# Kernel tuning notes

Measured on AMD Instinct MI355X. Metric: run time of the kernel, lower is better.

Reference implementation:

```python
import jax, jax.numpy as jnp
import numpy as np
import math

D_MODEL = 512
D_STATE = 16
D_CONV = 4
EXPAND = 2
D_INNER = D_MODEL * EXPAND
B, L = 2, 2048
EPS = 1e-8


def setup_inputs() -> dict:
    key = jax.random.key(0)
    ks = jax.random.split(key, 10)
    s_in = 1.0 / math.sqrt(D_MODEL)
    s_x = 1.0 / math.sqrt(D_INNER)
    s_c = 1.0 / math.sqrt(D_CONV)
    return {
        "x": jax.random.normal(ks[0], (B, L, D_MODEL), jnp.float32),
        "W_in": jax.random.uniform(ks[1], (D_MODEL, 2 * D_INNER), jnp.float32, -s_in, s_in),
        "b_in": jax.random.uniform(ks[2], (2 * D_INNER,), jnp.float32, -s_in, s_in),
        "conv_w": jax.random.uniform(ks[3], (D_INNER, 1, D_CONV), jnp.float32, -s_c, s_c),
        "conv_b": jax.random.uniform(ks[4], (D_INNER,), jnp.float32, -s_c, s_c),
        "W_x": jax.random.uniform(ks[5], (D_INNER, 2 * D_STATE + 1), jnp.float32, -s_x, s_x),
        "b_x": jax.random.uniform(ks[6], (2 * D_STATE + 1,), jnp.float32, -s_x, s_x),
        "A_log": jax.random.uniform(ks[7], (D_STATE,), jnp.float32, -math.log(D_STATE), -1.0),
        "D": jnp.ones((D_INNER,), jnp.float32),
        "W_out": jax.random.uniform(ks[8], (D_INNER, D_MODEL), jnp.float32, -s_x, s_x),
        "b_out": jax.random.uniform(ks[9], (D_MODEL,), jnp.float32, -s_x, s_x),
    }


def _silu(v):
    return v * jax.nn.sigmoid(v)


def _causal_depthwise_conv(x_blc, conv_w, conv_b):
    # x_blc: (B, L, D_inner); conv_w: (D_inner, 1, K). Torch pads K-1 both sides
    # then slices [:L] == causal left pad of K-1.
    lhs = jnp.transpose(x_blc, (0, 2, 1))  # (B, C, L)
    out = jax.lax.conv_general_dilated(
        lhs, conv_w,
        window_strides=(1,),
        padding=[(D_CONV - 1, 0)],
        dimension_numbers=("NCH", "OIH", "NCH"),
        feature_group_count=D_INNER,
    )
    out = out + conv_b[None, :, None]
    return jnp.transpose(out, (0, 2, 1))  # (B, L, C)


def reference(x, W_in, b_in, conv_w, conv_b, W_x, b_x, A_log, D, W_out, b_out):
    # in_proj and split
    xr = x @ W_in + b_in                      # (B, L, 2*Di)
    x_inner, res = jnp.split(xr, 2, axis=-1)  # each (B, L, Di)

    xc = _silu(_causal_depthwise_conv(x_inner, conv_w, conv_b))  # (B, L, Di)

    # selective scan (cumprod/cumsum formulation, faithful to source)
    BCdt = xc @ W_x + b_x                     # (B, L, 2S+1)
    B_sel = BCdt[..., :D_STATE]               # (B, L, S)
    C_sel = BCdt[..., D_STATE:2 * D_STATE]    # (B, L, S)
    dt = jax.nn.softplus(BCdt[..., -1:])      # (B, L, 1)

    A = -jnp.exp(A_log)                       # (S,)
    A_bar = jnp.exp(dt * A[None, None, :])    # (B, L, S)
    P = jnp.maximum(jnp.cumprod(A_bar, axis=1), EPS)  # (B, L, S)

    u = B_sel[..., None] * xc[:, :, None, :]  # (B, L, S, Di)
    g = jnp.cumsum(u / P[..., None], axis=1)  # (B, L, S, Di)
    h = g * P[..., None]                      # (B, L, S, Di)
    y = jnp.einsum("bls,blsd->bld", C_sel, h) + D[None, None, :] * xc

    y = y * _silu(res)
    return y @ W_out + b_out
```

## Files before the change

### kernel.cpp

```cpp
#include <hip/hip_runtime.h>
#include <hip/hip_bf16.h>
#include <cmath>


#define L_SEQ 2048
#define NBATCH 2
#define DI 1024
#define NC 64
#define LC 32
#define EPS_F 1e-8f
#define LOG_EPS -18.420680744f

typedef __attribute__((ext_vector_type(8))) __bf16 bf16x8;
typedef __attribute__((ext_vector_type(4))) float f32x4;

__device__ __forceinline__ float silu_f(float v) {
    return v / (1.f + __expf(-v));
}

__device__ __forceinline__ ushort bf16_bits(float v) {
    __hip_bfloat16 h = __float2bfloat16(v);
    return *reinterpret_cast<ushort*>(&h);
}

__device__ __forceinline__ float bf2f(ushort u) {
    union { unsigned u; float f; } c;
    c.u = ((unsigned)u) << 16;
    return c.f;
}

__global__ __launch_bounds__(256) void gemm1_mfma(
    const ushort* __restrict__ A, const ushort* __restrict__ Bt,
    const float* __restrict__ bias, ushort* __restrict__ C0,
    ushort* __restrict__ C1, int M, int N, int K)
{
    __shared__ ushort lA[128 * 64];
    __shared__ ushort lB[128 * 64];
    const int tid = threadIdx.x;
    const int w = tid >> 6, ln = tid & 63;
    const int wr = w >> 1, wc = w & 1;
    const int bm = blockIdx.y * 128, bn = blockIdx.x * 128;
    const int q = ln >> 4, r = ln & 15;
    f32x4 acc[4][4] = {};

    for (int k0 = 0; k0 < K; k0 += 64) {
        #pragma unroll
        for (int j = 0; j < 4; ++j) {
            int i = (w * 4 + j) * 64 + ln;
            int m = i >> 3, k8 = (i & 7) * 8;
            __builtin_amdgcn_global_load_lds(
                (const __attribute__((address_space(1))) void*)(A + (size_t)(bm + m) * K + k0 + k8),
                (__attribute__((address_space(3))) void*)(lA + (size_t)i * 8),
                16, 0, 0);
            __builtin_amdgcn_global_load_lds(
                (const __attribute__((address_space(1))) void*)(Bt + (size_t)(bn + m) * K + k0 + k8),
                (__attribute__((address_space(3))) void*)(lB + (size_t)i * 8),
                16, 0, 0);
        }
        __syncthreads();
        #pragma unroll
        for (int kk = 0; kk < 2; ++kk) {
            const int ko = kk * 32 + q * 8;
            bf16x8 af[4], bfr[4];
            #pragma unroll
            for (int m = 0; m < 4; ++m)
                af[m] = *reinterpret_cast<const bf16x8*>(&lA[(wr * 64 + m * 16 + r) * 64 + ko]);
            #pragma unroll
            for (int n = 0; n < 4; ++n)
                bfr[n] = *reinterpret_cast<const bf16x8*>(&lB[(wc * 64 + n * 16 + r) * 64 + ko]);
            #pragma unroll
            for (int m = 0; m < 4; ++m)
                #pragma unroll
                for (int n = 0; n < 4; ++n)
                    acc[m][n] = __builtin_amdgcn_mfma_f32_16x16x32_bf16(af[m], bfr[n], acc[m][n], 0, 0, 0);
        }
        __syncthreads();
    }

    const bool lo = (bn < 1024);
    #pragma unroll
    for (int n = 0; n < 4; ++n) {
        int col = bn + wc * 64 + n * 16 + r;
        float bv = bias[col];
        #pragma unroll
        for (int m = 0; m < 4; ++m) {
            int row0 = bm + wr * 64 + m * 16 + q * 4;
            #pragma unroll
            for (int j = 0; j < 4; ++j) {
                ushort v = bf16_bits(acc[m][n][j] + bv);
                if (lo) C0[(size_t)(row0 + j) * 1024 + col];
                if (lo) C0[(size_t)(row0 + j) * 1024 + col] = v;
                else    C1[(size_t)(row0 + j) * 1024 + (col - 1024)] = v;
            }
        }
    }
}

__global__ __launch_bounds__(256) void gemm2_mfma(
    const ushort* __restrict__ A, const ushort* __restrict__ Bt,
    const float* __restrict__ bias, float* __restrict__ C,
    int M, int N, int K)
{
    __shared__ ushort lA[128 * 64];
    __shared__ ushort lB[64 * 64];
    const int tid = threadIdx.x;
    const int w = tid >> 6, ln = tid & 63;
    const int wr = w >> 1, wc = w & 1;
    const int bm = blockIdx.y * 128, bn = blockIdx.x * 64;
    const int q = ln >> 4, r = ln & 15;
    f32x4 acc[4][2] = {};

    for (int k0 = 0; k0 < K; k0 += 64) {
        #pragma unroll
        for (int j = 0; j < 4; ++j) {
            int i = (w * 4 + j) * 64 + ln;
            int m = i >> 3, k8 = (i & 7) * 8;
            __builtin_amdgcn_global_load_lds(
                (const __attribute__((address_space(1))) void*)(A + (size_t)(bm + m) * K + k0 + k8),
                (__attribute__((address_space(3))) void*)(lA + (size_t)i * 8),
                16, 0, 0);
        }
        #pragma unroll
        for (int j = 0; j < 2; ++j) {
            int i = (w * 2 + j) * 64 + ln;
            int m = i >> 3, k8 = (i & 7) * 8;
            __builtin_amdgcn_global_load_lds(
                (const __attribute__((address_space(1))) void*)(Bt + (size_t)(bn + m) * K + k0 + k8),
                (__attribute__((address_space(3))) void*)(lB + (size_t)i * 8),
                16, 0, 0);
        }
        __syncthreads();
        #pragma unroll
        for (int kk = 0; kk < 2; ++kk) {
            const int ko = kk * 32 + q * 8;
            bf16x8 af[4], bfr[2];
            #pragma unroll
            for (int m = 0; m < 4; ++m)
                af[m] = *reinterpret_cast<const bf16x8*>(&lA[(wr * 64 + m * 16 + r) * 64 + ko]);
            #pragma unroll
            for (int n = 0; n < 2; ++n)
                bfr[n] = *reinterpret_cast<const bf16x8*>(&lB[(wc * 32 + n * 16 + r) * 64 + ko]);
            #pragma unroll
            for (int m = 0; m < 4; ++m)
                #pragma unroll
                for (int n = 0; n < 2; ++n)
                    acc[m][n] = __builtin_amdgcn_mfma_f32_16x16x32_bf16(af[m], bfr[n], acc[m][n], 0, 0, 0);
        }
        __syncthreads();
    }

    #pragma unroll
    for (int n = 0; n < 2; ++n) {
        int col = bn + wc * 32 + n * 16 + r;
        float bv = bias[col];
        #pragma unroll
        for (int m = 0; m < 4; ++m) {
            int row0 = bm + wr * 64 + m * 16 + q * 4;
            #pragma unroll
            for (int j = 0; j < 4; ++j)
                C[(size_t)(row0 + j) * N + col] = acc[m][n][j] + bv;
        }
    }
}

__global__ __launch_bounds__(256) void gemm3_mfma(
    const ushort* __restrict__ A, const ushort* __restrict__ Bt,
    float* __restrict__ P)
{
    __shared__ ushort lA[64 * 64];
    __shared__ ushort lB[48 * 64];
    const int t = threadIdx.x;
    const int w = t >> 6, ln = t & 63;
    const int q = ln >> 4, r = ln & 15;
    const int bm = blockIdx.y * 64;
    const int ks = blockIdx.x;
    f32x4 acc[3] = {};

    for (int k0 = ks * 256; k0 < ks * 256 + 256; k0 += 64) {
        #pragma unroll
        for (int j = 0; j < 2; ++j) {
            int i = (w * 2 + j) * 64 + ln;
            int m = i >> 3, k8 = (i & 7) * 8;
            __builtin_amdgcn_global_load_lds(
                (const __attribute__((address_space(1))) void*)(A + (size_t)(bm + m) * 1024 + k0 + k8),
                (__attribute__((address_space(3))) void*)(lA + (size_t)i * 8),
                16, 0, 0);
        }
        #pragma unroll
        for (int p = 0; p < 2; ++p) {
            int cidx = p * 4 + w;
            if (cidx < 6) {
                int i = cidx * 64 + ln;
                int m = i >> 3, k8 = (i & 7) * 8;
                __builtin_amdgcn_global_load_lds(
                    (const __attribute__((address_space(1))) void*)(Bt + (size_t)m * 1024 + k0 + k8),
                    (__attribute__((address_space(3))) void*)(lB + (size_t)i * 8),
                    16, 0, 0);
            }
        }
        __syncthreads();
        #pragma unroll
        for (int kk = 0; kk < 2; ++kk) {
            const int ko = kk * 32 + q * 8;
            bf16x8 af = *reinterpret_cast<const bf16x8*>(&lA[(w * 16 + r) * 64 + ko]);
            #pragma unroll
            for (int n = 0; n < 3; ++n) {
                bf16x8 bf = *reinterpret_cast<const bf16x8*>(&lB[(n * 16 + r) * 64 + ko]);
                acc[n] = __builtin_amdgcn_mfma_f32_16x16x32_bf16(af, bf, acc[n], 0, 0, 0);
            }
        }
        __syncthreads();
    }

    const int row0 = bm + w * 16 + q * 4;
    const size_t base = (size_t)ks * 196608;
    #pragma unroll
    for (int n = 0; n < 3; ++n)
        #pragma unroll
        for (int j = 0; j < 4; ++j)
            P[base + (size_t)(row0 + j) * 48 + n * 16 + r] = acc[n][j];
}

__global__ __launch_bounds__(256) void gemm3_reduce(
    const float* __restrict__ P, const float* __restrict__ b_x,
    float* __restrict__ scal)
{
    int idx = blockIdx.x * 256 + threadIdx.x;
    int l = idx / 48, c = idx - l * 48;
    if (c >= 33) return;
    float v = b_x[c] + P[idx] + P[idx + 196608] + P[idx + 393216] + P[idx + 589824];
    scal[(size_t)l * 48 + c] = v;
}

__global__ __launch_bounds__(256) void prep_all(
    const float* __restrict__ x, const float* __restrict__ W_in,
    const float* __restrict__ W_out, const float* __restrict__ W_x,
    ushort* __restrict__ xbf, ushort* __restrict__ Wt1,
    ushort* __restrict__ Wt2, ushort* __restrict__ Wxt)
{
    const int bid = blockIdx.x;
    const int t = threadIdx.x;
    if (bid < 2048) {
        int i = bid * 256 + t;
        float4 v = reinterpret_cast<const float4*>(x)[i];
        ushort4 o;
        o.x = bf16_bits(v.x); o.y = bf16_bits(v.y);
        o.z = bf16_bits(v.z); o.w = bf16_bits(v.w);
        reinterpret_cast<ushort4*>(xbf)[i] = o;
        return;
    }
    if (bid >= 2432) {
        int idx = (bid - 2432) * 256 + t;
        int c = idx >> 10, k = idx & 1023;
        Wxt[idx] = (c < 33) ? bf16_bits(W_x[(size_t)k * 33 + c]) : (ushort)0;
        return;
    }
    __shared__ float ld[64][65];
    const float* src; ushort* dst; int R, C, tile;
    if (bid < 2304) { src = W_in;  dst = Wt1; R = 512;  C = 2048; tile = bid - 2048; }
    else            { src = W_out; dst = Wt2; R = 1024; C = 512;  tile = bid - 2304; }
    const int ctiles = C / 64;
    const int r0 = (tile / ctiles) * 64, c0 = (tile % ctiles) * 64;
    #pragma unroll
    for (int i = 0; i < 16; ++i) {
        int idx = t + i * 256;
        int rr = idx >> 6, cc = idx & 63;
        ld[rr][cc] = src[(size_t)(r0 + rr) * C + c0 + cc];
    }
    __syncthreads();
    #pragma unroll
    for (int i = 0; i < 16; ++i) {
        int idx = t + i * 256;
        int cc = idx >> 6, rr = idx & 63;
        dst[(size_t)(c0 + cc) * R + r0 + rr] = bf16_bits(ld[rr][cc]);
    }
}

__global__ __launch_bounds__(256) void conv_silu(
    const ushort* __restrict__ xinb, const float* __restrict__ cw,
    const float* __restrict__ cb, ushort* __restrict__ xcb)
{
    int idx = blockIdx.x * 256 + threadIdx.x;
    int d = idx & (DI - 1);
    int l = (idx >> 10) & (L_SEQ - 1);
    float4 w = *reinterpret_cast<const float4*>(cw + d * 4);
    float acc = cb[d];
    long base = (long)idx;
    if (l >= 3) acc = fmaf(bf2f(xinb[base - 3 * 1024]), w.x, acc);
    if (l >= 2) acc = fmaf(bf2f(xinb[base - 2 * 1024]), w.y, acc);
    if (l >= 1) acc = fmaf(bf2f(xinb[base - 1 * 1024]), w.z, acc);
    acc = fmaf(bf2f(xinb[base]), w.w, acc);
    xcb[idx] = bf16_bits(silu_f(acc));
}

__global__ __launch_bounds__(256) void rates_par(
    float* __restrict__ scal, const float* __restrict__ A_log,
    float* __restrict__ RP)
{
    int b = blockIdx.x;
    int t = threadIdx.x;
    __shared__ float cdt[L_SEQ];
    __shared__ float wsum[4];
    __shared__ float An[16];
    if (t < 16) An[t] = -__expf(A_log[t]);
    float* base = scal + (long)b * L_SEQ * 48;

    float dt[8];
    float run = 0.f;
    const int l0 = t * 8;
    #pragma unroll
    for (int i = 0; i < 8; ++i) {
        float raw = base[(l0 + i) * 48 + 32];
        float d = (raw > 20.f) ? raw : log1pf(__expf(raw));
        dt[i] = d;
        run += d;
        cdt[l0 + i] = run;
    }

    float x = run;
    int lane = t & 63;
    #pragma unroll
    for (int d = 1; d < 64; d <<= 1) {
        float v = __shfl_up(x, d, 64);
        if (lane >= d) x += v;
    }
    int w = t >> 6;
    if (lane == 63) wsum[w] = x;
    __syncthreads();
    float woff = 0.f;
    for (int i = 0; i < w; ++i) woff += wsum[i];
    float toff = woff + x - run;
    #pragma unroll
    for (int i = 0; i < 8; ++i) cdt[l0 + i] += toff;
    __syncthreads();

    float cprev = (l0 == 0) ? 0.f : cdt[l0 - 1];
    #pragma unroll
    for (int i = 0; i < 8; ++i) {
        int l = l0 + i;
        float cl = cdt[l];
        float rv[16];
        #pragma unroll
        for (int s = 0; s < 16; ++s) {
            float A = An[s];
            float rr;
            if (A * cl >= LOG_EPS) {
                rr = __expf(A * dt[i]);
            } else {
                float lp = A * cprev;
                rr = (lp >= LOG_EPS) ? EPS_F / __expf(lp) : 1.f;
            }
            rv[s] = rr;
        }
        float4* dst = reinterpret_cast<float4*>(base + l * 48 + 32);
        dst[0] = *reinterpret_cast<float4*>(&rv[0]);
        dst[1] = *reinterpret_cast<float4*>(&rv[4]);
        dst[2] = *reinterpret_cast<float4*>(&rv[8]);
        dst[3] = *reinterpret_cast<float4*>(&rv[12]);
        cprev = cl;
    }

    if ((t & 3) == 3) {
        int c = t >> 2;
        float ce = cdt[c * LC + LC - 1];
        float cp = (c == 0) ? 0.f : cdt[c * LC - 1];
        for (int s = 0; s < 16; ++s) {
            float A = An[s];
            float pe = fmaxf(__expf(A * ce), EPS_F);
            float pp = fmaxf(__expf(A * cp), EPS_F);
            RP[(b * NC + c) * 16 + s] = pe / pp;
        }
    }
}

__global__ __launch_bounds__(128) void scan_states(
    const float* __restrict__ scal, const ushort* __restrict__ xcb,
    ushort* __restrict__ Sbf)
{
    int b = blockIdx.z, c = blockIdx.y;
    int d = blockIdx.x * 128 + threadIdx.x;
    __shared__ float sc[LC * 48];
    const float4* src = reinterpret_cast<const float4*>(scal + ((long)(b * L_SEQ) + c * LC) * 48);
    float4* dst = reinterpret_cast<float4*>(sc);
    for (int i = threadIdx.x; i < LC * 48 / 4; i += 128) dst[i] = src[i];

    const ushort* xcp = xcb + ((long)(b * L_SEQ) + c * LC) * 1024 + d;
    float xv[LC];
    #pragma unroll
    for (int ll = 0; ll < LC; ++ll) xv[ll] = bf2f(xcp[(long)ll * 1024]);
    __syncthreads();

    float h[16];
    #pragma unroll
    for (int s = 0; s < 16; ++s) h[s] = 0.f;
    #pragma unroll
    for (int ll = 0; ll < LC; ++ll) {
        const float* e = sc + ll * 48;
        #pragma unroll
        for (int s = 0; s < 16; ++s) h[s] = fmaf(e[32 + s], h[s], e[s] * xv[ll]);
    }
    ushort* Sp = Sbf + ((long)(b * NC + c) * 16) * 1024 + d;
    #pragma unroll
    for (int s = 0; s < 16; ++s) Sp[(long)s * 1024] = bf16_bits(h[s]);
}

__global__ __launch_bounds__(256) void stitch(
    ushort* __restrict__ Sbf, const float* __restrict__ RP)
{
    const int tid = threadIdx.x;
    const int idx = blockIdx.x * 256 + tid;
    const int b = blockIdx.y;
    const int d = idx & 1023, s = idx >> 10;
    __shared__ float rps[NC];
    if (tid < NC) rps[tid] = RP[(b * NC + tid) * 16 + s];

    const long base = ((long)(b * NC) * 16 + s) * 1024 + d;
    const long cs = 16 * 1024;
    float v[NC];
    #pragma unroll
    for (int c = 0; c < NC; ++c) v[c] = bf2f(Sbf[base + c * cs]);
    __syncthreads();
    float H = 0.f;
    #pragma unroll
    for (int c = 0; c < NC; ++c) {
        float tmp = v[c];
        v[c] = H;
        H = fmaf(rps[c], H, tmp);
    }
    #pragma unroll
    for (int c = 0; c < NC; ++c) Sbf[base + c * cs] = bf16_bits(v[c]);
}

__global__ __launch_bounds__(128) void scan_out(
    const float* __restrict__ scal, const ushort* __restrict__ xcb,
    const ushort* __restrict__ Hin, const float* __restrict__ Dw,
    const ushort* __restrict__ resb, ushort* __restrict__ ybf)
{
    int b = blockIdx.z, c = blockIdx.y;
    int d = blockIdx.x * 128 + threadIdx.x;
    __shared__ float sc[LC * 48];
    const float4* src = reinterpret_cast<const float4*>(scal + ((long)(b * L_SEQ) + c * LC) * 48);
    float4* dst = reinterpret_cast<float4*>(sc);
    for (int i = threadIdx.x; i < LC * 48 / 4; i += 128) dst[i] = src[i];

    const long row0 = (long)(b * L_SEQ) + c * LC;
    float xv[LC], rv[LC];
    #pragma unroll
    for (int ll = 0; ll < LC; ++ll) xv[ll] = bf2f(xcb[(row0 + ll) * 1024 + d]);
    #pragma unroll
    for (int ll = 0; ll < LC; ++ll) rv[ll] = bf2f(resb[(row0 + ll) * 1024 + d]);
    float h[16];
    long hoff = ((long)(b * NC + c) * 16) * 1024 + d;
    #pragma unroll
    for (int s = 0; s < 16; ++s) h[s] = bf2f(Hin[hoff + (long)s * 1024]);
    __syncthreads();

    float Dd = Dw[d];
    #pragma unroll
    for (int ll = 0; ll < LC; ++ll) {
        const float* e = sc + ll * 48;
        float y = 0.f;
        #pragma unroll
        for (int s = 0; s < 16; ++s) {
            h[s] = fmaf(e[32 + s], h[s], e[s] * xv[ll]);
            y = fmaf(e[16 + s], h[s], y);
        }
        y = fmaf(Dd, xv[ll], y);
        ybf[(row0 + ll) * 1024 + d] = bf16_bits(y * silu_f(rv[ll]));
    }
}

extern "C" void kernel_launch(void* const* d_in, const int* in_sizes, int n_in,
                              void* d_out, int out_size, void* d_ws, size_t ws_size,
                              hipStream_t stream)
{
    const float* x      = (const float*)d_in[0];
    const float* W_in   = (const float*)d_in[1];
    const float* b_in   = (const float*)d_in[2];
    const float* conv_w = (const float*)d_in[3];
    const float* conv_b = (const float*)d_in[4];
    const float* W_x    = (const float*)d_in[5];
    const float* b_x    = (const float*)d_in[6];
    const float* A_log  = (const float*)d_in[7];
    const float* Dw     = (const float*)d_in[8];
    const float* W_out  = (const float*)d_in[9];
    const float* b_out  = (const float*)d_in[10];
    float* out = (float*)d_out;

    ushort* u    = (ushort*)d_ws;
    ushort* xinb = u;
    ushort* resb = xinb + 4194304;
    ushort* xcb  = resb + 4194304;
    ushort* Sbf  = xcb + 4194304;
    ushort* xbf  = Sbf + 2097152;
    ushort* Wt1  = xbf + 2097152;
    ushort* Wt2  = Wt1 + 1048576;
    ushort* Wxt  = Wt2 + 524288;
    ushort* ybf  = Wxt + 49152;
    float* scal  = (float*)(ybf + 4194304);
    float* RP    = scal + 196608;
    float* P     = RP + 2048;

    prep_all<<<2624, 256, 0, stream>>>(x, W_in, W_out, W_x, xbf, Wt1, Wt2, Wxt);

    gemm1_mfma<<<dim3(2048 / 128, 4096 / 128), 256, 0, stream>>>(
        xbf, Wt1, b_in, xinb, resb, 4096, 2048, 512);

    conv_silu<<<(NBATCH * L_SEQ * DI) / 256, 256, 0, stream>>>(xinb, conv_w, conv_b, xcb);

    gemm3_mfma<<<dim3(4, 4096 / 64), 256, 0, stream>>>(xcb, Wxt, P);
    gemm3_reduce<<<196608 / 256, 256, 0, stream>>>(P, b_x, scal);

    rates_par<<<NBATCH, 256, 0, stream>>>(scal, A_log, RP);

    scan_states<<<dim3(DI / 128, NC, NBATCH), 128, 0, stream>>>(scal, xcb, Sbf);
    stitch<<<dim3(64, NBATCH), 256, 0, stream>>>(Sbf, RP);
    scan_out<<<dim3(DI / 128, NC, NBATCH), 128, 0, stream>>>(scal, xcb, Sbf, Dw, resb, ybf);

    gemm2_mfma<<<dim3(512 / 64, 4096 / 128), 256, 0, stream>>>(
        ybf, Wt2, b_out, out, 4096, 512, 1024);
}
```

Before: 116.1 us.

## Fuse scan stages into cooperative kernel and merge split-K reduce into rates

Merges the split-K partial-sum reduction of the x-projection into the rates kernel: the dt column is summed directly from the partials, and the B/C columns are reduced by the extra blocks. The three scan kernels (chunk states, cross-chunk stitch, output) become one cooperative kernel separated by grid-wide syncs, so xv and the shared-memory scalars stay resident across phases. This is meant to cut launch overhead and redundant reloads. The cost is two grid barriers, a stitch phase that runs on only 256 of the 1024 blocks, and a requirement that all 1024 blocks be co-resident. It also drops a stray dead load in gemm1's epilogue.

```diff
diff --git a/kernel.cpp b/kernel.cpp
--- a/kernel.cpp
+++ b/kernel.cpp
@@ -1,6 +1,9 @@
 #include <hip/hip_runtime.h>
 #include <hip/hip_bf16.h>
+#include <hip/hip_cooperative_groups.h>
 #include <cmath>
+
+namespace cg = cooperative_groups;
 
 
 #define L_SEQ 2048
@@ -88,7 +91,6 @@
             #pragma unroll
             for (int j = 0; j < 4; ++j) {
                 ushort v = bf16_bits(acc[m][n][j] + bv);
-                if (lo) C0[(size_t)(row0 + j) * 1024 + col];
                 if (lo) C0[(size_t)(row0 + j) * 1024 + col] = v;
                 else    C1[(size_t)(row0 + j) * 1024 + (col - 1024)] = v;
             }
@@ -219,17 +221,6 @@
         #pragma unroll
         for (int j = 0; j < 4; ++j)
             P[base + (size_t)(row0 + j) * 48 + n * 16 + r] = acc[n][j];
-}
-
-__global__ __launch_bounds__(256) void gemm3_reduce(
-    const float* __restrict__ P, const float* __restrict__ b_x,
-    float* __restrict__ scal)
-{
-    int idx = blockIdx.x * 256 + threadIdx.x;
-    int l = idx / 48, c = idx - l * 48;
-    if (c >= 33) return;
-    float v = b_x[c] + P[idx] + P[idx + 196608] + P[idx + 393216] + P[idx + 589824];
-    scal[(size_t)l * 48 + c] = v;
 }
 
 __global__ __launch_bounds__(256) void prep_all(
@@ -293,24 +284,39 @@
     xcb[idx] = bf16_bits(silu_f(acc));
 }
 
-__global__ __launch_bounds__(256) void rates_par(
+__global__ __launch_bounds__(256) void rates_fused(
+    const float* __restrict__ P, const float* __restrict__ b_x,
     float* __restrict__ scal, const float* __restrict__ A_log,
     float* __restrict__ RP)
 {
-    int b = blockIdx.x;
-    int t = threadIdx.x;
+    const int bid = blockIdx.x;
+    const int t = threadIdx.x;
+
+    if (bid >= 2) {
+        int idx = (bid - 2) * 256 + t;
+        int l = idx >> 5, c = idx & 31;
+        int pi = l * 48 + c;
+        float v = b_x[c] + P[pi] + P[pi + 196608] + P[pi + 393216] + P[pi + 589824];
+        scal[(size_t)l * 48 + c] = v;
+        return;
+    }
+
+    const int b = bid;
     __shared__ float cdt[L_SEQ];
     __shared__ float wsum[4];
     __shared__ float An[16];
     if (t < 16) An[t] = -__expf(A_log[t]);
     float* base = scal + (long)b * L_SEQ * 48;
+    const float bdt = b_x[32];
 
     float dt[8];
     float run = 0.f;
     const int l0 = t * 8;
     #pragma unroll
     for (int i = 0; i < 8; ++i) {
-        float raw = base[(l0 + i) * 48 + 32];
+        int gl = b * L_SEQ + l0 + i;
+        int pi = gl * 48 + 32;
+        float raw = bdt + P[pi] + P[pi + 196608] + P[pi + 393216] + P[pi + 589824];
         float d = (raw > 20.f) ? raw : log1pf(__expf(raw));
         dt[i] = d;
         run += d;
@@ -373,89 +379,79 @@
     }
 }
 
-__global__ __launch_bounds__(128) void scan_states(
+__global__ __launch_bounds__(128, 2) void scan3(
     const float* __restrict__ scal, const ushort* __restrict__ xcb,
-    ushort* __restrict__ Sbf)
-{
-    int b = blockIdx.z, c = blockIdx.y;
-    int d = blockIdx.x * 128 + threadIdx.x;
+    const ushort* __restrict__ resb, const float* __restrict__ RP,
+    const float* __restrict__ Dw, ushort* Sbf, ushort* __restrict__ ybf)
+{
+    cg::grid_group grid = cg::this_grid();
+    const int bx = blockIdx.x;
+    const int dblk = bx & 7, c = (bx >> 3) & (NC - 1), b = bx >> 9;
+    const int d = dblk * 128 + threadIdx.x;
+
     __shared__ float sc[LC * 48];
     const float4* src = reinterpret_cast<const float4*>(scal + ((long)(b * L_SEQ) + c * LC) * 48);
-    float4* dst = reinterpret_cast<float4*>(sc);
-    for (int i = threadIdx.x; i < LC * 48 / 4; i += 128) dst[i] = src[i];
-
-    const ushort* xcp = xcb + ((long)(b * L_SEQ) + c * LC) * 1024 + d;
+    float4* dst4 = reinterpret_cast<float4*>(sc);
+    for (int i = threadIdx.x; i < LC * 48 / 4; i += 128) dst4[i] = src[i];
+
+    const long row0 = (long)(b * L_SEQ) + c * LC;
     float xv[LC];
     #pragma unroll
-    for (int ll = 0; ll < LC; ++ll) xv[ll] = bf2f(xcp[(long)ll * 1024]);
+    for (int ll = 0; ll < LC; ++ll) xv[ll] = bf2f(xcb[(row0 + ll) * 1024 + d]);
     __syncthreads();
 
-    float h[16];
-    #pragma unroll
-    for (int s = 0; s < 16; ++s) h[s] = 0.f;
-    #pragma unroll
-    for (int ll = 0; ll < LC; ++ll) {
-        const float* e = sc + ll * 48;
-        #pragma unroll
-        for (int s = 0; s < 16; ++s) h[s] = fmaf(e[32 + s], h[s], e[s] * xv[ll]);
-    }
-    ushort* Sp = Sbf + ((long)(b * NC + c) * 16) * 1024 + d;
-    #pragma unroll
-    for (int s = 0; s < 16; ++s) Sp[(long)s * 1024] = bf16_bits(h[s]);
-}
-
-__global__ __launch_bounds__(256) void stitch(
-    ushort* __restrict__ Sbf, const float* __restrict__ RP)
-{
-    const int tid = threadIdx.x;
-    const int idx = blockIdx.x * 256 + tid;
-    const int b = blockIdx.y;
-    const int d = idx & 1023, s = idx >> 10;
-    __shared__ float rps[NC];
-    if (tid < NC) rps[tid] = RP[(b * NC + tid) * 16 + s];
-
-    const long base = ((long)(b * NC) * 16 + s) * 1024 + d;
-    const long cs = 16 * 1024;
-    float v[NC];
-    #pragma unroll
-    for (int c = 0; c < NC; ++c) v[c] = bf2f(Sbf[base + c * cs]);
-    __syncthreads();
-    float H = 0.f;
-    #pragma unroll
-    for (int c = 0; c < NC; ++c) {
-        float tmp = v[c];
-        v[c] = H;
-        H = fmaf(rps[c], H, tmp);
-    }
-    #pragma unroll
-    for (int c = 0; c < NC; ++c) Sbf[base + c * cs] = bf16_bits(v[c]);
-}
-
-__global__ __launch_bounds__(128) void scan_out(
-    const float* __restrict__ scal, const ushort* __restrict__ xcb,
-    const ushort* __restrict__ Hin, const float* __restrict__ Dw,
-    const ushort* __restrict__ resb, ushort* __restrict__ ybf)
-{
-    int b = blockIdx.z, c = blockIdx.y;
-    int d = blockIdx.x * 128 + threadIdx.x;
-    __shared__ float sc[LC * 48];
-    const float4* src = reinterpret_cast<const float4*>(scal + ((long)(b * L_SEQ) + c * LC) * 48);
-    float4* dst = reinterpret_cast<float4*>(sc);
-    for (int i = threadIdx.x; i < LC * 48 / 4; i += 128) dst[i] = src[i];
-
-    const long row0 = (long)(b * L_SEQ) + c * LC;
-    float xv[LC], rv[LC];
-    #pragma unroll
-    for (int ll = 0; ll < LC; ++ll) xv[ll] = bf2f(xcb[(row0 + ll) * 1024 + d]);
+    {
+        float h[16];
+        #pragma unroll
+        for (int s = 0; s < 16; ++s) h[s] = 0.f;
+        #pragma unroll
+        for (int ll = 0; ll < LC; ++ll) {
+            const float* e = sc + ll * 48;
+            #pragma unroll
+            for (int s = 0; s < 16; ++s) h[s] = fmaf(e[32 + s], h[s], e[s] * xv[ll]);
+        }
+        ushort* Sp = Sbf + ((long)(b * NC + c) * 16) * 1024 + d;
+        #pragma unroll
+        for (int s = 0; s < 16; ++s) Sp[(long)s * 1024] = bf16_bits(h[s]);
+    }
+
+    grid.sync();
+
+    if (bx < 256) {
+        int idx = bx * 128 + (int)threadIdx.x;
+        int b2 = idx >> 14;
+        int s2 = (idx >> 10) & 15;
+        int d2 = idx & 1023;
+        const long sbase = ((long)(b2 * NC) * 16 + s2) * 1024 + d2;
+        const long cs = 16 * 1024;
+        float H = 0.f;
+        #pragma unroll
+        for (int g = 0; g < NC / 8; ++g) {
+            float v[8];
+            #pragma unroll
+            for (int k = 0; k < 8; ++k) v[k] = bf2f(Sbf[sbase + (long)(g * 8 + k) * cs]);
+            #pragma unroll
+            for (int k = 0; k < 8; ++k) {
+                int c2 = g * 8 + k;
+                float tmp = v[k];
+                Sbf[sbase + (long)c2 * cs] = bf16_bits(H);
+                H = fmaf(RP[(b2 * NC + c2) * 16 + s2], H, tmp);
+            }
+        }
+    }
+
+    grid.sync();
+
+    float rv[LC];
     #pragma unroll
     for (int ll = 0; ll < LC; ++ll) rv[ll] = bf2f(resb[(row0 + ll) * 1024 + d]);
     float h[16];
-    long hoff = ((long)(b * NC + c) * 16) * 1024 + d;
-    #pragma unroll
-    for (int s = 0; s < 16; ++s) h[s] = bf2f(Hin[hoff + (long)s * 1024]);
-    __syncthreads();
-
-    float Dd = Dw[d];
+    {
+        const ushort* Hp = Sbf + ((long)(b * NC + c) * 16) * 1024 + d;
+        #pragma unroll
+        for (int s = 0; s < 16; ++s) h[s] = bf2f(Hp[(long)s * 1024]);
+    }
+    const float Dd = Dw[d];
     #pragma unroll
     for (int ll = 0; ll < LC; ++ll) {
         const float* e = sc + ll * 48;
@@ -509,13 +505,15 @@
     conv_silu<<<(NBATCH * L_SEQ * DI) / 256, 256, 0, stream>>>(xinb, conv_w, conv_b, xcb);
 
     gemm3_mfma<<<dim3(4, 4096 / 64), 256, 0, stream>>>(xcb, Wxt, P);
-    gemm3_reduce<<<196608 / 256, 256, 0, stream>>>(P, b_x, scal);
-
-    rates_par<<<NBATCH, 256, 0, stream>>>(scal, A_log, RP);
-
-    scan_states<<<dim3(DI / 128, NC, NBATCH), 128, 0, stream>>>(scal, xcb, Sbf);
-    stitch<<<dim3(64, NBATCH), 256, 0, stream>>>(Sbf, RP);
-    scan_out<<<dim3(DI / 128, NC, NBATCH), 128, 0, stream>>>(scal, xcb, Sbf, Dw, resb, ybf);
+
+    rates_fused<<<514, 256, 0, stream>>>(P, b_x, scal, A_log, RP);
+
+    {
+        void* args[] = {(void*)&scal, (void*)&xcb, (void*)&resb, (void*)&RP,
+                        (void*)&Dw, (void*)&Sbf, (void*)&ybf};
+        hipLaunchCooperativeKernel((void*)scan3, dim3(1024), dim3(128),
+                                   args, 0, stream);
+    }
 
     gemm2_mfma<<<dim3(512 / 64, 4096 / 128), 256, 0, stream>>>(
         ybf, Wt2, b_out, out, 4096, 512, 1024);
```

After: 375.5 us. +223.3%, slower.

## Fuse causal conv+SiLU into the x_proj MFMA GEMM with 8-way K split

Applied to the files above, without the earlier changes.

Replaces the separate conv_silu kernel and gemm3 with one kernel. It loads a 67-row halo of xinb plus a 128-wide K slice of Wxt into LDS, computes the depthwise conv and SiLU in shared memory, writes xcb out, and runs the MFMA partial GEMM from LDS. This removes one kernel launch and the round trip of xcb through global memory before the GEMM. In exchange, the K split goes from 4 to 8, so the reduce kernel reads twice as many partials and the P workspace doubles. A dead load in gemm1's epilogue is also removed.

```diff
diff --git a/kernel.cpp b/kernel.cpp
--- a/kernel.cpp
+++ b/kernel.cpp
@@ -88,7 +88,6 @@
             #pragma unroll
             for (int j = 0; j < 4; ++j) {
                 ushort v = bf16_bits(acc[m][n][j] + bv);
-                if (lo) C0[(size_t)(row0 + j) * 1024 + col];
                 if (lo) C0[(size_t)(row0 + j) * 1024 + col] = v;
                 else    C1[(size_t)(row0 + j) * 1024 + (col - 1024)] = v;
             }
@@ -163,53 +162,70 @@
     }
 }
 
-__global__ __launch_bounds__(256) void gemm3_mfma(
-    const ushort* __restrict__ A, const ushort* __restrict__ Bt,
-    float* __restrict__ P)
-{
-    __shared__ ushort lA[64 * 64];
-    __shared__ ushort lB[48 * 64];
+__global__ __launch_bounds__(256) void conv_gemm3(
+    const ushort* __restrict__ xinb, const float* __restrict__ cw,
+    const float* __restrict__ cb, const ushort* __restrict__ Wxt,
+    ushort* __restrict__ xcb, float* __restrict__ P)
+{
+    __shared__ ushort sxin[67 * 128];
+    __shared__ ushort sxc[64 * 128];
+    __shared__ ushort swx[48 * 128];
+    __shared__ float  scw[128][4];
+    __shared__ float  scb[128];
+
     const int t = threadIdx.x;
+    const int ks = blockIdx.x, rt = blockIdx.y;
+    const int bm = rt * 64;
+    const int kb = ks * 128;
+    const int l0 = bm & (L_SEQ - 1);
+
+    for (int i = t; i < 67 * 16; i += 256) {
+        int rr = i >> 4, c8 = (i & 15) * 8;
+        uint4 v = {0, 0, 0, 0};
+        if (l0 + rr - 3 >= 0)
+            v = *reinterpret_cast<const uint4*>(&xinb[(size_t)(bm + rr - 3) * 1024 + kb + c8]);
+        *reinterpret_cast<uint4*>(&sxin[rr * 128 + c8]) = v;
+    }
+    for (int i = t; i < 48 * 16; i += 256) {
+        int rr = i >> 4, c8 = (i & 15) * 8;
+        *reinterpret_cast<uint4*>(&swx[rr * 128 + c8]) =
+            *reinterpret_cast<const uint4*>(&Wxt[(size_t)rr * 1024 + kb + c8]);
+    }
+    for (int i = t; i < 512; i += 256) scw[i >> 2][i & 3] = cw[(size_t)(kb + (i >> 2)) * 4 + (i & 3)];
+    if (t < 128) scb[t] = cb[kb + t];
+    __syncthreads();
+
+    for (int i = t; i < 1024; i += 256) {
+        int row = i >> 4, c8 = (i & 15) * 8;
+        ushort ov[8];
+        #pragma unroll
+        for (int j = 0; j < 8; ++j) {
+            int col = c8 + j;
+            float a = scb[col];
+            a = fmaf(bf2f(sxin[(row + 0) * 128 + col]), scw[col][0], a);
+            a = fmaf(bf2f(sxin[(row + 1) * 128 + col]), scw[col][1], a);
+            a = fmaf(bf2f(sxin[(row + 2) * 128 + col]), scw[col][2], a);
+            a = fmaf(bf2f(sxin[(row + 3) * 128 + col]), scw[col][3], a);
+            ov[j] = bf16_bits(silu_f(a));
+        }
+        *reinterpret_cast<uint4*>(&sxc[row * 128 + c8]) = *reinterpret_cast<uint4*>(ov);
+        *reinterpret_cast<uint4*>(&xcb[(size_t)(bm + row) * 1024 + kb + c8]) =
+            *reinterpret_cast<uint4*>(ov);
+    }
+    __syncthreads();
+
     const int w = t >> 6, ln = t & 63;
     const int q = ln >> 4, r = ln & 15;
-    const int bm = blockIdx.y * 64;
-    const int ks = blockIdx.x;
     f32x4 acc[3] = {};
-
-    for (int k0 = ks * 256; k0 < ks * 256 + 256; k0 += 64) {
-        #pragma unroll
-        for (int j = 0; j < 2; ++j) {
-            int i = (w * 2 + j) * 64 + ln;
-            int m = i >> 3, k8 = (i & 7) * 8;
-            __builtin_amdgcn_global_load_lds(
-                (const __attribute__((address_space(1))) void*)(A + (size_t)(bm + m) * 1024 + k0 + k8),
-                (__attribute__((address_space(3))) void*)(lA + (size_t)i * 8),
-                16, 0, 0);
-        }
-        #pragma unroll
-        for (int p = 0; p < 2; ++p) {
-            int cidx = p * 4 + w;
-            if (cidx < 6) {
-                int i = cidx * 64 + ln;
-                int m = i >> 3, k8 = (i & 7) * 8;
-                __builtin_amdgcn_global_load_lds(
-                    (const __attribute__((address_space(1))) void*)(Bt + (size_t)m * 1024 + k0 + k8),
-                    (__attribute__((address_space(3))) void*)(lB + (size_t)i * 8),
-                    16, 0, 0);
-            }
-        }
-        __syncthreads();
-        #pragma unroll
-        for (int kk = 0; kk < 2; ++kk) {
-            const int ko = kk * 32 + q * 8;
-            bf16x8 af = *reinterpret_cast<const bf16x8*>(&lA[(w * 16 + r) * 64 + ko]);
-            #pragma unroll
-            for (int n = 0; n < 3; ++n) {
-                bf16x8 bf = *reinterpret_cast<const bf16x8*>(&lB[(n * 16 + r) * 64 + ko]);
-                acc[n] = __builtin_amdgcn_mfma_f32_16x16x32_bf16(af, bf, acc[n], 0, 0, 0);
-            }
-        }
-        __syncthreads();
+    #pragma unroll
+    for (int kk = 0; kk < 4; ++kk) {
+        const int ko = kk * 32 + q * 8;
+        bf16x8 af = *reinterpret_cast<const bf16x8*>(&sxc[(w * 16 + r) * 128 + ko]);
+        #pragma unroll
+        for (int n = 0; n < 3; ++n) {
+            bf16x8 bf = *reinterpret_cast<const bf16x8*>(&swx[(n * 16 + r) * 128 + ko]);
+            acc[n] = __builtin_amdgcn_mfma_f32_16x16x32_bf16(af, bf, acc[n], 0, 0, 0);
+        }
     }
 
     const int row0 = bm + w * 16 + q * 4;
@@ -228,7 +244,9 @@
     int idx = blockIdx.x * 256 + threadIdx.x;
     int l = idx / 48, c = idx - l * 48;
     if (c >= 33) return;
-    float v = b_x[c] + P[idx] + P[idx + 196608] + P[idx + 393216] + P[idx + 589824];
+    float v = b_x[c];
+    #pragma unroll
+    for (int k = 0; k < 8; ++k) v += P[idx + k * 196608];
     scal[(size_t)l * 48 + c] = v;
 }
 
@@ -274,23 +292,6 @@
         int cc = idx >> 6, rr = idx & 63;
         dst[(size_t)(c0 + cc) * R + r0 + rr] = bf16_bits(ld[rr][cc]);
     }
-}
-
-__global__ __launch_bounds__(256) void conv_silu(
-    const ushort* __restrict__ xinb, const float* __restrict__ cw,
-    const float* __restrict__ cb, ushort* __restrict__ xcb)
-{
-    int idx = blockIdx.x * 256 + threadIdx.x;
-    int d = idx & (DI - 1);
-    int l = (idx >> 10) & (L_SEQ - 1);
-    float4 w = *reinterpret_cast<const float4*>(cw + d * 4);
-    float acc = cb[d];
-    long base = (long)idx;
-    if (l >= 3) acc = fmaf(bf2f(xinb[base - 3 * 1024]), w.x, acc);
-    if (l >= 2) acc = fmaf(bf2f(xinb[base - 2 * 1024]), w.y, acc);
-    if (l >= 1) acc = fmaf(bf2f(xinb[base - 1 * 1024]), w.z, acc);
-    acc = fmaf(bf2f(xinb[base]), w.w, acc);
-    xcb[idx] = bf16_bits(silu_f(acc));
 }
 
 __global__ __launch_bounds__(256) void rates_par(
@@ -506,10 +507,9 @@
     gemm1_mfma<<<dim3(2048 / 128, 4096 / 128), 256, 0, stream>>>(
         xbf, Wt1, b_in, xinb, resb, 4096, 2048, 512);
 
-    conv_silu<<<(NBATCH * L_SEQ * DI) / 256, 256, 0, stream>>>(xinb, conv_w, conv_b, xcb);
-
-    gemm3_mfma<<<dim3(4, 4096 / 64), 256, 0, stream>>>(xcb, Wxt, P);
-    gemm3_reduce<<<196608 / 256, 256, 0, stream>>>(P, b_x, scal);
+    conv_gemm3<<<dim3(8, 64), 256, 0, stream>>>(xinb, conv_w, conv_b, Wxt, xcb, P);
+
+    gemm3_reduce<<<768, 256, 0, stream>>>(P, b_x, scal);
 
     rates_par<<<NBATCH, 256, 0, stream>>>(scal, A_log, RP);
 
```

Result: faster. 109.7 us (-5.6%).
